# Performance work log

Measured on AMD Instinct MI355X. Metric: run time of the kernel, lower is better.

Reference implementation:

```python
import jax, jax.numpy as jnp
import numpy as np

N_NODES = 50000
N_EDGES = 800000
IN_CH = 64
HID = 64
HID2 = HID // 2  # 32


def _sage_conv(x, src, dst, w_l, w_r, b, n_nodes):
    """PyG SAGEConv (aggr='mean', root_weight=True):
    out = lin_l(mean_{j in N(i)} x_j) + lin_r(x_i), bias in lin_l.
    Messages flow src -> dst (source_to_target)."""
    msg = x[src]  # [E, d] gather of source features
    summed = jax.ops.segment_sum(msg, dst, num_segments=n_nodes)  # [N, d]
    cnt = jax.ops.segment_sum(jnp.ones((src.shape[0],), x.dtype), dst,
                              num_segments=n_nodes)  # [N]
    mean = summed / jnp.maximum(cnt, 1.0)[:, None]
    return mean @ w_l + b + x @ w_r


def setup_inputs() -> dict:
    key = jax.random.key(0)
    ks = jax.random.split(key, 12)
    s = 0.05
    x = jax.random.normal(ks[0], (N_NODES, IN_CH), dtype=jnp.float32)
    edge_index = jax.random.randint(ks[1], (2, N_EDGES), 0, N_NODES, dtype=jnp.int32)
    return {
        "x": x,
        "edge_index": edge_index,
        # SAGEConv layer 1 (in -> hidden)
        "w1_l": jax.random.normal(ks[2], (IN_CH, HID), dtype=jnp.float32) * s,
        "w1_r": jax.random.normal(ks[3], (IN_CH, HID), dtype=jnp.float32) * s,
        "b1": jnp.zeros((HID,), jnp.float32),
        # SAGEConv layer 2 (hidden -> hidden//2)
        "w2_l": jax.random.normal(ks[4], (HID, HID2), dtype=jnp.float32) * s,
        "w2_r": jax.random.normal(ks[5], (HID, HID2), dtype=jnp.float32) * s,
        "b2": jnp.zeros((HID2,), jnp.float32),
        # classifier MLP: Linear(32,16) -> ReLU -> Linear(16,2)
        "wc1": jax.random.normal(ks[6], (HID2, 16), dtype=jnp.float32) * s,
        "bc1": jnp.zeros((16,), jnp.float32),
        "wc2": jax.random.normal(ks[7], (16, 2), dtype=jnp.float32) * s,
        "bc2": jnp.zeros((2,), jnp.float32),
    }


def reference(x, edge_index, w1_l, w1_r, b1, w2_l, w2_r, b2, wc1, bc1, wc2, bc2):
    src, dst = edge_index[0], edge_index[1]
    n = x.shape[0]
    # Dropout is identity in eval / deterministic reference.
    h = jax.nn.relu(_sage_conv(x, src, dst, w1_l, w1_r, b1, n))
    h = jax.nn.relu(_sage_conv(h, src, dst, w2_l, w2_r, b2, n))
    h = jax.nn.relu(h @ wc1 + bc1)
    out = h @ wc2 + bc2  # [N, 2]
    return out
```

## Files before the change

### kernel.cpp

```cpp
#include <hip/hip_runtime.h>
#include <hip/hip_fp16.h>

#define N_NODES 50000
#define N_EDGES 800000
#define NBINS   391
#define CAP     4096
#define EPB     4096
#define NBLK_E  ((N_EDGES + EPB - 1) / EPB)
#define NTILE   391
#define LSTRIDE 129

__global__ __launch_bounds__(512) void k_binA(const int* __restrict__ src,
                                              const int* __restrict__ dst,
                                              int* __restrict__ bincur,
                                              int* __restrict__ binned) {
    __shared__ int cnt[NBINS];
    __shared__ int sc[512];
    __shared__ int lpos[NBINS];
    __shared__ int base[NBINS];
    __shared__ int stage[EPB];
    __shared__ unsigned short sbin[EPB];
    int t = threadIdx.x;
    int blkbase = blockIdx.x * EPB;
    int nE = min(EPB, N_EDGES - blkbase);
    for (int i = t; i < NBINS; i += 512) cnt[i] = 0;
    __syncthreads();
    int sv[8], dv[8];
#pragma unroll
    for (int k = 0; k < 8; ++k) {
        int e = blkbase + t + k * 512;
        if (e < N_EDGES) {
            sv[k] = src[e];
            dv[k] = dst[e];
            atomicAdd(&cnt[dv[k] >> 7], 1);
        } else dv[k] = -1;
    }
    __syncthreads();
    sc[t] = (t < NBINS) ? cnt[t] : 0;
    __syncthreads();
    for (int d = 1; d < 512; d <<= 1) {
        int add = (t >= d) ? sc[t - d] : 0;
        __syncthreads();
        sc[t] += add;
        __syncthreads();
    }
    for (int b = t; b < NBINS; b += 512) {
        int excl = sc[b] - cnt[b];
        lpos[b] = excl;
        sc[b] = excl;
        if (cnt[b] > 0) base[b] = b * CAP + atomicAdd(&bincur[b], cnt[b]);
    }
    __syncthreads();
#pragma unroll
    for (int k = 0; k < 8; ++k) {
        if (dv[k] >= 0) {
            int b = dv[k] >> 7;
            int p = atomicAdd(&lpos[b], 1);
            stage[p] = (sv[k] & 0xFFFF) | ((dv[k] & 127) << 16);
            sbin[p] = (unsigned short)b;
        }
    }
    __syncthreads();
    for (int i = t; i < nE; i += 512) {
        int b = sbin[i];
        int pos = base[b] + (i - sc[b]);
        if (pos < (b + 1) * CAP) binned[pos] = stage[i];
    }
}

__global__ __launch_bounds__(512) void k_binB_pre1(
        const int* __restrict__ bincur, int* __restrict__ binned,
        int* __restrict__ off, unsigned short* __restrict__ deg,
        int* __restrict__ esrc,
        const float* __restrict__ x,
        const float* __restrict__ wl, const float* __restrict__ wr,
        const float* __restrict__ b,
        __half* __restrict__ ph, float* __restrict__ q) {
    __shared__ float smem[64 * LSTRIDE];
    int t = threadIdx.x;
    int bb = blockIdx.x;
    if (bb < NBINS) {
        int* buf = (int*)smem;
        int* cnt = buf + CAP;
        int* tmp = cnt + 128;
        int* cur = tmp + 128;
        int n0 = bb << 7;
        int seg0 = bb * CAP;
        int n = min(bincur[bb], CAP);
        if (t < 128) cnt[t] = 0;
        __syncthreads();
        for (int i = t; i < n; i += 512) atomicAdd(&cnt[binned[seg0 + i] >> 16], 1);
        __syncthreads();
        int v = (t < 128) ? cnt[t] : 0;
        if (t < 128) tmp[t] = v;
        __syncthreads();
        int val = v;
        for (int d = 1; d < 128; d <<= 1) {
            int add = (t >= d && t < 128) ? tmp[t - d] : 0;
            __syncthreads();
            if (t < 128) { val += add; tmp[t] = val; }
            __syncthreads();
        }
        if (t < 128) {
            int excl = val - v;
            cur[t] = excl;
            int node = n0 + t;
            if (node < N_NODES) {
                off[node] = seg0 + excl;
                deg[node] = (unsigned short)v;
            }
        }
        __syncthreads();
        for (int i = t; i < n; i += 512) {
            int w = binned[seg0 + i];
            int p = atomicAdd(&cur[w >> 16], 1);
            buf[p] = w & 0xFFFF;
        }
        __syncthreads();
        for (int i = t; i < n; i += 512) esrc[seg0 + i] = buf[i];
        return;
    }
    float* sx = smem;
    int g0 = (bb - NBINS) * 128;
#pragma unroll
    for (int i = 0; i < 4; ++i) {
        int f = t + i * 512;
        int nd = f >> 4, cq = f & 15;
        int gn = g0 + nd;
        float4 v = (gn < N_NODES) ? ((const float4*)x)[(size_t)gn * 16 + cq]
                                  : make_float4(0.f, 0.f, 0.f, 0.f);
        sx[(cq * 4 + 0) * LSTRIDE + nd] = v.x;
        sx[(cq * 4 + 1) * LSTRIDE + nd] = v.y;
        sx[(cq * 4 + 2) * LSTRIDE + nd] = v.z;
        sx[(cq * 4 + 3) * LSTRIDE + nd] = v.w;
    }
    __syncthreads();
    int role = __builtin_amdgcn_readfirstlane(t >> 7);
    int wsel = role >> 1;
    int c0 = (role & 1) * 32;
    int ln = t & 127;
    int node = g0 + ln;
    const float* __restrict__ wm = wsel ? wr : wl;
    float acc[32];
    if (wsel) {
#pragma unroll
        for (int c = 0; c < 32; ++c) acc[c] = b[c0 + c];
    } else {
#pragma unroll
        for (int c = 0; c < 32; ++c) acc[c] = 0.f;
    }
#pragma unroll
    for (int k = 0; k < 64; ++k) {
        float xk = sx[k * LSTRIDE + ln];
#pragma unroll
        for (int c = 0; c < 32; ++c)
            acc[c] = fmaf(xk, wm[k * 64 + c0 + c], acc[c]);
    }
    if (node >= N_NODES) return;
    if (wsel == 0) {
        alignas(16) __half2 hv[16];
#pragma unroll
        for (int i = 0; i < 16; ++i)
            hv[i] = __floats2half2_rn(acc[2 * i], acc[2 * i + 1]);
        float4* op = (float4*)(ph + (size_t)node * 64 + c0);
#pragma unroll
        for (int i = 0; i < 4; ++i) op[i] = ((float4*)hv)[i];
    } else {
        float4* op = (float4*)(q + (size_t)node * 64 + c0);
#pragma unroll
        for (int i = 0; i < 8; ++i)
            op[i] = make_float4(acc[4 * i], acc[4 * i + 1], acc[4 * i + 2], acc[4 * i + 3]);
    }
}

__device__ __forceinline__ void acc8(float* a, float4 rv) {
    const __half2* hp = (const __half2*)&rv;
    float2 f0 = __half22float2(hp[0]), f1 = __half22float2(hp[1]);
    float2 f2 = __half22float2(hp[2]), f3 = __half22float2(hp[3]);
    a[0] += f0.x; a[1] += f0.y; a[2] += f1.x; a[3] += f1.y;
    a[4] += f2.x; a[5] += f2.y; a[6] += f3.x; a[7] += f3.y;
}

__global__ __launch_bounds__(1024) void k_agg1_pre2(
        const int* __restrict__ off, const unsigned short* __restrict__ deg,
        const int* __restrict__ esrc,
        const __half* __restrict__ ph, const float* __restrict__ q,
        const float* __restrict__ w2l, const float* __restrict__ w2r,
        const float* __restrict__ b2,
        __half* __restrict__ zh, float* __restrict__ r) {
    __shared__ float sx[64 * LSTRIDE];
    int t = threadIdx.x;
    int n0 = blockIdx.x << 7;
    int half = t >> 5;
    int l32 = t & 31;
    int eg = l32 >> 3;
    int cg = l32 & 7;
    for (int p = 0; p < 4; ++p) {
        int nl = half + 32 * p;
        int node = n0 + nl;
        if (node < N_NODES) {
            int s0 = off[node];
            int dv = deg[node];
            int s1 = s0 + dv;
            float a0[8] = {0,0,0,0,0,0,0,0}, a1[8] = {0,0,0,0,0,0,0,0};
            float a2[8] = {0,0,0,0,0,0,0,0}, a3[8] = {0,0,0,0,0,0,0,0};
            for (int i = s0; i < s1; i += 16) {
                int i0 = i + eg, i1 = i + 4 + eg, i2 = i + 8 + eg, i3 = i + 12 + eg;
                if (i0 < s1) acc8(a0, *(const float4*)(ph + (size_t)esrc[i0] * 64 + (cg << 3)));
                if (i1 < s1) acc8(a1, *(const float4*)(ph + (size_t)esrc[i1] * 64 + (cg << 3)));
                if (i2 < s1) acc8(a2, *(const float4*)(ph + (size_t)esrc[i2] * 64 + (cg << 3)));
                if (i3 < s1) acc8(a3, *(const float4*)(ph + (size_t)esrc[i3] * 64 + (cg << 3)));
            }
#pragma unroll
            for (int j = 0; j < 8; ++j) a0[j] += a1[j] + (a2[j] + a3[j]);
#pragma unroll
            for (int j = 0; j < 8; ++j) {
                a0[j] += __shfl_xor(a0[j], 8);
                a0[j] += __shfl_xor(a0[j], 16);
            }
            if (eg == 0) {
                float inv = 1.0f / fmaxf((float)dv, 1.0f);
                const float4* qp = (const float4*)(q + (size_t)node * 64 + (cg << 3));
                float4 q0 = qp[0], q1 = qp[1];
                float* d = sx + (cg << 3) * LSTRIDE + nl;
                d[0 * LSTRIDE] = fmaxf(fmaf(a0[0], inv, q0.x), 0.f);
                d[1 * LSTRIDE] = fmaxf(fmaf(a0[1], inv, q0.y), 0.f);
                d[2 * LSTRIDE] = fmaxf(fmaf(a0[2], inv, q0.z), 0.f);
                d[3 * LSTRIDE] = fmaxf(fmaf(a0[3], inv, q0.w), 0.f);
                d[4 * LSTRIDE] = fmaxf(fmaf(a0[4], inv, q1.x), 0.f);
                d[5 * LSTRIDE] = fmaxf(fmaf(a0[5], inv, q1.y), 0.f);
                d[6 * LSTRIDE] = fmaxf(fmaf(a0[6], inv, q1.z), 0.f);
                d[7 * LSTRIDE] = fmaxf(fmaf(a0[7], inv, q1.w), 0.f);
            }
        }
    }
    __syncthreads();
    int g = __builtin_amdgcn_readfirstlane(t >> 7);
    int role = g & 1;
    int c0 = (g >> 1) * 8;
    int ln = t & 127;
    int node = n0 + ln;
    const float* __restrict__ wm = role ? w2r : w2l;
    float acc[8];
    if (role) {
#pragma unroll
        for (int c = 0; c < 8; ++c) acc[c] = b2[c0 + c];
    } else {
#pragma unroll
        for (int c = 0; c < 8; ++c) acc[c] = 0.f;
    }
#pragma unroll
    for (int k = 0; k < 64; ++k) {
        float xk = sx[k * LSTRIDE + ln];
#pragma unroll
        for (int c = 0; c < 8; ++c)
            acc[c] = fmaf(xk, wm[k * 32 + c0 + c], acc[c]);
    }
    if (node >= N_NODES) return;
    if (role == 0) {
        alignas(16) __half2 hv[4];
#pragma unroll
        for (int i = 0; i < 4; ++i)
            hv[i] = __floats2half2_rn(acc[2 * i], acc[2 * i + 1]);
        *(float4*)(zh + (size_t)node * 32 + c0) = *(float4*)hv;
    } else {
        float4* op = (float4*)(r + (size_t)node * 32 + c0);
        op[0] = make_float4(acc[0], acc[1], acc[2], acc[3]);
        op[1] = make_float4(acc[4], acc[5], acc[6], acc[7]);
    }
}

__global__ __launch_bounds__(256) void k_agg2cls(const int* __restrict__ off,
                                                 const unsigned short* __restrict__ deg,
                                                 const int* __restrict__ esrc,
                                                 const __half* __restrict__ zh,
                                                 const float* __restrict__ r,
                                                 const float* __restrict__ wc1,
                                                 const float* __restrict__ bc1,
                                                 const float* __restrict__ wc2,
                                                 const float* __restrict__ bc2,
                                                 float* __restrict__ out) {
    __shared__ float sh2[16 * 33];
    __shared__ float sh3[16 * 17];
    __shared__ float swc1[512];
    __shared__ float sbc1[16];
    __shared__ float swc2[32];
    __shared__ float sbc2[2];
    int t = threadIdx.x;
    swc1[t] = wc1[t];
    swc1[t + 256] = wc1[t + 256];
    if (t < 16) sbc1[t] = bc1[t];
    if (t < 32) swc2[t] = wc2[t];
    if (t < 2)  sbc2[t] = bc2[t];

    int lane = t & 63;
    int l16 = lane & 15;
    int nl = (t >> 4) & 15;
    int node = blockIdx.x * 16 + nl;
    int eg = l16 >> 2;
    int cg = l16 & 3;
    int s0 = off[node];
    int dv = deg[node];
    int s1 = s0 + dv;
    float a0[8] = {0,0,0,0,0,0,0,0}, a1[8] = {0,0,0,0,0,0,0,0};
    float a2[8] = {0,0,0,0,0,0,0,0}, a3[8] = {0,0,0,0,0,0,0,0};
    for (int i = s0; i < s1; i += 16) {
        int i0 = i + eg, i1 = i + 4 + eg, i2 = i + 8 + eg, i3 = i + 12 + eg;
        if (i0 < s1) acc8(a0, *(const float4*)(zh + (size_t)esrc[i0] * 32 + (cg << 3)));
        if (i1 < s1) acc8(a1, *(const float4*)(zh + (size_t)esrc[i1] * 32 + (cg << 3)));
        if (i2 < s1) acc8(a2, *(const float4*)(zh + (size_t)esrc[i2] * 32 + (cg << 3)));
        if (i3 < s1) acc8(a3, *(const float4*)(zh + (size_t)esrc[i3] * 32 + (cg << 3)));
    }
#pragma unroll
    for (int j = 0; j < 8; ++j) a0[j] += a1[j] + (a2[j] + a3[j]);
#pragma unroll
    for (int j = 0; j < 8; ++j) {
        a0[j] += __shfl_xor(a0[j], 4);
        a0[j] += __shfl_xor(a0[j], 8);
    }
    if (eg == 0) {
        float inv = 1.0f / fmaxf((float)dv, 1.0f);
        const float4* rp = (const float4*)(r + (size_t)node * 32 + (cg << 3));
        float4 r0 = rp[0], r1 = rp[1];
        float* d = sh2 + nl * 33 + (cg << 3);
        d[0] = fmaxf(fmaf(a0[0], inv, r0.x), 0.f);
        d[1] = fmaxf(fmaf(a0[1], inv, r0.y), 0.f);
        d[2] = fmaxf(fmaf(a0[2], inv, r0.z), 0.f);
        d[3] = fmaxf(fmaf(a0[3], inv, r0.w), 0.f);
        d[4] = fmaxf(fmaf(a0[4], inv, r1.x), 0.f);
        d[5] = fmaxf(fmaf(a0[5], inv, r1.y), 0.f);
        d[6] = fmaxf(fmaf(a0[6], inv, r1.z), 0.f);
        d[7] = fmaxf(fmaf(a0[7], inv, r1.w), 0.f);
    }
    __syncthreads();
    int n = t >> 4, j = t & 15;
    float acc1 = sbc1[j];
#pragma unroll
    for (int k = 0; k < 32; ++k)
        acc1 = fmaf(sh2[n * 33 + k], swc1[k * 16 + j], acc1);
    sh3[n * 17 + j] = fmaxf(acc1, 0.f);
    __syncthreads();
    if (t < 16) {
        int nn = t;
        float o0 = sbc2[0], o1 = sbc2[1];
#pragma unroll
        for (int k = 0; k < 16; ++k) {
            float h3k = sh3[nn * 17 + k];
            o0 = fmaf(h3k, swc2[k * 2 + 0], o0);
            o1 = fmaf(h3k, swc2[k * 2 + 1], o1);
        }
        int gnode = blockIdx.x * 16 + nn;
        *(float2*)(out + (size_t)gnode * 2) = make_float2(o0, o1);
    }
}

extern "C" void kernel_launch(void* const* d_in, const int* in_sizes, int n_in,
                              void* d_out, int out_size, void* d_ws, size_t ws_size,
                              hipStream_t stream) {
    const float* x   = (const float*)d_in[0];
    const int*   ei  = (const int*)d_in[1];
    const int*   src = ei;
    const int*   dst = ei + N_EDGES;
    const float* w1l = (const float*)d_in[2];
    const float* w1r = (const float*)d_in[3];
    const float* b1  = (const float*)d_in[4];
    const float* w2l = (const float*)d_in[5];
    const float* w2r = (const float*)d_in[6];
    const float* b2  = (const float*)d_in[7];
    const float* wc1 = (const float*)d_in[8];
    const float* bc1 = (const float*)d_in[9];
    const float* wc2 = (const float*)d_in[10];
    const float* bc2 = (const float*)d_in[11];
    float* out = (float*)d_out;

    int*   wi     = (int*)d_ws;
    int*   bincur = wi;
    int*   binned = wi + 400;
    int*   esrc   = binned + (size_t)NBINS * CAP;
    int*   off    = esrc + (size_t)NBINS * CAP;
    unsigned short* deg = (unsigned short*)(off + N_NODES);
    float* q      = (float*)(deg + N_NODES + (N_NODES & 1));
    float* phf    = q + (size_t)64 * N_NODES;
    __half* ph    = (__half*)phf;
    float* zhf    = phf + (size_t)32 * N_NODES;
    __half* zh    = (__half*)zhf;
    float* r      = zhf + (size_t)16 * N_NODES;

    hipMemsetAsync(bincur, 0, 400 * sizeof(int), stream);
    k_binA<<<NBLK_E, 512, 0, stream>>>(src, dst, bincur, binned);

    k_binB_pre1<<<NBINS + NTILE, 512, 0, stream>>>(bincur, binned, off, deg, esrc,
                                                   x, w1l, w1r, b1, ph, q);

    k_agg1_pre2<<<NBINS, 1024, 0, stream>>>(off, deg, esrc, ph, q,
                                            w2l, w2r, b2, zh, r);

    k_agg2cls<<<N_NODES / 16, 256, 0, stream>>>(off, deg, esrc, zh, r,
                                                wc1, bc1, wc2, bc2, out);
}
```

Measured before the change: 187.5 us.

## Split layer-1 fp16 features into two 32-channel planes and gather per plane

The fp16 projected features are now stored as two separate planes of 32 channels each (64 bytes per node) instead of one 128-byte row. The aggregation kernel runs two phases, one per plane, so each phase's random gather touches a smaller working set that fits better in cache. Each node now gets 8 edges in flight per 32-lane group instead of 4. The cost is that the edge index list and offsets are read twice, plus an extra barrier and a three-step shuffle reduction per node.

```diff
diff --git a/kernel.cpp b/kernel.cpp
--- a/kernel.cpp
+++ b/kernel.cpp
@@ -75,7 +75,8 @@
         const float* __restrict__ x,
         const float* __restrict__ wl, const float* __restrict__ wr,
         const float* __restrict__ b,
-        __half* __restrict__ ph, float* __restrict__ q) {
+        __half* __restrict__ ph0, __half* __restrict__ ph1,
+        float* __restrict__ q) {
     __shared__ float smem[64 * LSTRIDE];
     int t = threadIdx.x;
     int bb = blockIdx.x;
@@ -162,7 +163,8 @@
 #pragma unroll
         for (int i = 0; i < 16; ++i)
             hv[i] = __floats2half2_rn(acc[2 * i], acc[2 * i + 1]);
-        float4* op = (float4*)(ph + (size_t)node * 64 + c0);
+        __half* plane = c0 ? ph1 : ph0;
+        float4* op = (float4*)(plane + (size_t)node * 32);
 #pragma unroll
         for (int i = 0; i < 4; ++i) op[i] = ((float4*)hv)[i];
     } else {
@@ -184,7 +186,8 @@
 __global__ __launch_bounds__(1024) void k_agg1_pre2(
         const int* __restrict__ off, const unsigned short* __restrict__ deg,
         const int* __restrict__ esrc,
-        const __half* __restrict__ ph, const float* __restrict__ q,
+        const __half* __restrict__ ph0, const __half* __restrict__ ph1,
+        const float* __restrict__ q,
         const float* __restrict__ w2l, const float* __restrict__ w2r,
         const float* __restrict__ b2,
         __half* __restrict__ zh, float* __restrict__ r) {
@@ -193,48 +196,51 @@
     int n0 = blockIdx.x << 7;
     int half = t >> 5;
     int l32 = t & 31;
-    int eg = l32 >> 3;
-    int cg = l32 & 7;
-    for (int p = 0; p < 4; ++p) {
-        int nl = half + 32 * p;
-        int node = n0 + nl;
-        if (node < N_NODES) {
-            int s0 = off[node];
-            int dv = deg[node];
-            int s1 = s0 + dv;
-            float a0[8] = {0,0,0,0,0,0,0,0}, a1[8] = {0,0,0,0,0,0,0,0};
-            float a2[8] = {0,0,0,0,0,0,0,0}, a3[8] = {0,0,0,0,0,0,0,0};
-            for (int i = s0; i < s1; i += 16) {
-                int i0 = i + eg, i1 = i + 4 + eg, i2 = i + 8 + eg, i3 = i + 12 + eg;
-                if (i0 < s1) acc8(a0, *(const float4*)(ph + (size_t)esrc[i0] * 64 + (cg << 3)));
-                if (i1 < s1) acc8(a1, *(const float4*)(ph + (size_t)esrc[i1] * 64 + (cg << 3)));
-                if (i2 < s1) acc8(a2, *(const float4*)(ph + (size_t)esrc[i2] * 64 + (cg << 3)));
-                if (i3 < s1) acc8(a3, *(const float4*)(ph + (size_t)esrc[i3] * 64 + (cg << 3)));
+    int eg = l32 >> 2;
+    int cg = l32 & 3;
+#pragma unroll
+    for (int phase = 0; phase < 2; ++phase) {
+        const __half* pp = phase ? ph1 : ph0;
+        for (int p = 0; p < 4; ++p) {
+            int nl = half + 32 * p;
+            int node = n0 + nl;
+            if (node < N_NODES) {
+                int s0 = off[node];
+                int dv = deg[node];
+                int s1 = s0 + dv;
+                float a0[8] = {0,0,0,0,0,0,0,0}, a1[8] = {0,0,0,0,0,0,0,0};
+                for (int i = s0; i < s1; i += 16) {
+                    int i0 = i + eg, i1 = i + 8 + eg;
+                    if (i0 < s1) acc8(a0, *(const float4*)(pp + (size_t)esrc[i0] * 32 + (cg << 3)));
+                    if (i1 < s1) acc8(a1, *(const float4*)(pp + (size_t)esrc[i1] * 32 + (cg << 3)));
+                }
+#pragma unroll
+                for (int j = 0; j < 8; ++j) a0[j] += a1[j];
+#pragma unroll
+                for (int j = 0; j < 8; ++j) {
+                    a0[j] += __shfl_xor(a0[j], 4);
+                    a0[j] += __shfl_xor(a0[j], 8);
+                    a0[j] += __shfl_xor(a0[j], 16);
+                }
+                if (eg == 0) {
+                    float inv = 1.0f / fmaxf((float)dv, 1.0f);
+                    int cb = phase * 32 + (cg << 3);
+                    const float4* qp = (const float4*)(q + (size_t)node * 64 + cb);
+                    float4 q0 = qp[0], q1 = qp[1];
+                    float* d = sx + cb * LSTRIDE + nl;
+                    d[0 * LSTRIDE] = fmaxf(fmaf(a0[0], inv, q0.x), 0.f);
+                    d[1 * LSTRIDE] = fmaxf(fmaf(a0[1], inv, q0.y), 0.f);
+                    d[2 * LSTRIDE] = fmaxf(fmaf(a0[2], inv, q0.z), 0.f);
+                    d[3 * LSTRIDE] = fmaxf(fmaf(a0[3], inv, q0.w), 0.f);
+                    d[4 * LSTRIDE] = fmaxf(fmaf(a0[4], inv, q1.x), 0.f);
+                    d[5 * LSTRIDE] = fmaxf(fmaf(a0[5], inv, q1.y), 0.f);
+                    d[6 * LSTRIDE] = fmaxf(fmaf(a0[6], inv, q1.z), 0.f);
+                    d[7 * LSTRIDE] = fmaxf(fmaf(a0[7], inv, q1.w), 0.f);
+                }
             }
-#pragma unroll
-            for (int j = 0; j < 8; ++j) a0[j] += a1[j] + (a2[j] + a3[j]);
-#pragma unroll
-            for (int j = 0; j < 8; ++j) {
-                a0[j] += __shfl_xor(a0[j], 8);
-                a0[j] += __shfl_xor(a0[j], 16);
-            }
-            if (eg == 0) {
-                float inv = 1.0f / fmaxf((float)dv, 1.0f);
-                const float4* qp = (const float4*)(q + (size_t)node * 64 + (cg << 3));
-                float4 q0 = qp[0], q1 = qp[1];
-                float* d = sx + (cg << 3) * LSTRIDE + nl;
-                d[0 * LSTRIDE] = fmaxf(fmaf(a0[0], inv, q0.x), 0.f);
-                d[1 * LSTRIDE] = fmaxf(fmaf(a0[1], inv, q0.y), 0.f);
-                d[2 * LSTRIDE] = fmaxf(fmaf(a0[2], inv, q0.z), 0.f);
-                d[3 * LSTRIDE] = fmaxf(fmaf(a0[3], inv, q0.w), 0.f);
-                d[4 * LSTRIDE] = fmaxf(fmaf(a0[4], inv, q1.x), 0.f);
-                d[5 * LSTRIDE] = fmaxf(fmaf(a0[5], inv, q1.y), 0.f);
-                d[6 * LSTRIDE] = fmaxf(fmaf(a0[6], inv, q1.z), 0.f);
-                d[7 * LSTRIDE] = fmaxf(fmaf(a0[7], inv, q1.w), 0.f);
-            }
-        }
-    }
-    __syncthreads();
+        }
+        __syncthreads();
+    }
     int g = __builtin_amdgcn_readfirstlane(t >> 7);
     int role = g & 1;
     int c0 = (g >> 1) * 8;
@@ -380,9 +386,11 @@
     int*   off    = esrc + (size_t)NBINS * CAP;
     unsigned short* deg = (unsigned short*)(off + N_NODES);
     float* q      = (float*)(deg + N_NODES + (N_NODES & 1));
-    float* phf    = q + (size_t)64 * N_NODES;
-    __half* ph    = (__half*)phf;
-    float* zhf    = phf + (size_t)32 * N_NODES;
+    float* p0f    = q + (size_t)64 * N_NODES;
+    __half* ph0   = (__half*)p0f;
+    float* p1f    = p0f + (size_t)16 * N_NODES;
+    __half* ph1   = (__half*)p1f;
+    float* zhf    = p1f + (size_t)16 * N_NODES;
     __half* zh    = (__half*)zhf;
     float* r      = zhf + (size_t)16 * N_NODES;
 
@@ -390,9 +398,9 @@
     k_binA<<<NBLK_E, 512, 0, stream>>>(src, dst, bincur, binned);
 
     k_binB_pre1<<<NBINS + NTILE, 512, 0, stream>>>(bincur, binned, off, deg, esrc,
-                                                   x, w1l, w1r, b1, ph, q);
-
-    k_agg1_pre2<<<NBINS, 1024, 0, stream>>>(off, deg, esrc, ph, q,
+                                                   x, w1l, w1r, b1, ph0, ph1, q);
+
+    k_agg1_pre2<<<NBINS, 1024, 0, stream>>>(off, deg, esrc, ph0, ph1, q,
                                             w2l, w2r, b2, zh, r);
 
     k_agg2cls<<<N_NODES / 16, 256, 0, stream>>>(off, deg, esrc, zh, r,
```

Measured after the change: 203.1 us. +8.3%, slower.

## Fuse first-layer projection into edge binning kernel, split bin finalize out

Applied to the files above, without the earlier changes.

The layer-1 dense projection (x@W_l, x@W_r) moves from the bin-finalize kernel into the first binning kernel as extra blocks, and bin finalize becomes its own kernel. The projection work now overlaps with the edge counting and scatter pass instead of with the per-bin sort. The intent is to balance the two launches better, since the binning pass is short and light on compute. The number of launches stays the same, and the binning blocks now reserve the larger shared-memory footprint of the projection, which may lower their occupancy.

```diff
diff --git a/kernel.cpp b/kernel.cpp
--- a/kernel.cpp
+++ b/kernel.cpp
@@ -10,68 +10,9 @@
 #define NTILE   391
 #define LSTRIDE 129
 
-__global__ __launch_bounds__(512) void k_binA(const int* __restrict__ src,
-                                              const int* __restrict__ dst,
-                                              int* __restrict__ bincur,
-                                              int* __restrict__ binned) {
-    __shared__ int cnt[NBINS];
-    __shared__ int sc[512];
-    __shared__ int lpos[NBINS];
-    __shared__ int base[NBINS];
-    __shared__ int stage[EPB];
-    __shared__ unsigned short sbin[EPB];
-    int t = threadIdx.x;
-    int blkbase = blockIdx.x * EPB;
-    int nE = min(EPB, N_EDGES - blkbase);
-    for (int i = t; i < NBINS; i += 512) cnt[i] = 0;
-    __syncthreads();
-    int sv[8], dv[8];
-#pragma unroll
-    for (int k = 0; k < 8; ++k) {
-        int e = blkbase + t + k * 512;
-        if (e < N_EDGES) {
-            sv[k] = src[e];
-            dv[k] = dst[e];
-            atomicAdd(&cnt[dv[k] >> 7], 1);
-        } else dv[k] = -1;
-    }
-    __syncthreads();
-    sc[t] = (t < NBINS) ? cnt[t] : 0;
-    __syncthreads();
-    for (int d = 1; d < 512; d <<= 1) {
-        int add = (t >= d) ? sc[t - d] : 0;
-        __syncthreads();
-        sc[t] += add;
-        __syncthreads();
-    }
-    for (int b = t; b < NBINS; b += 512) {
-        int excl = sc[b] - cnt[b];
-        lpos[b] = excl;
-        sc[b] = excl;
-        if (cnt[b] > 0) base[b] = b * CAP + atomicAdd(&bincur[b], cnt[b]);
-    }
-    __syncthreads();
-#pragma unroll
-    for (int k = 0; k < 8; ++k) {
-        if (dv[k] >= 0) {
-            int b = dv[k] >> 7;
-            int p = atomicAdd(&lpos[b], 1);
-            stage[p] = (sv[k] & 0xFFFF) | ((dv[k] & 127) << 16);
-            sbin[p] = (unsigned short)b;
-        }
-    }
-    __syncthreads();
-    for (int i = t; i < nE; i += 512) {
-        int b = sbin[i];
-        int pos = base[b] + (i - sc[b]);
-        if (pos < (b + 1) * CAP) binned[pos] = stage[i];
-    }
-}
-
-__global__ __launch_bounds__(512) void k_binB_pre1(
-        const int* __restrict__ bincur, int* __restrict__ binned,
-        int* __restrict__ off, unsigned short* __restrict__ deg,
-        int* __restrict__ esrc,
+__global__ __launch_bounds__(512) void k_binA_pre1(
+        const int* __restrict__ src, const int* __restrict__ dst,
+        int* __restrict__ bincur, int* __restrict__ binned,
         const float* __restrict__ x,
         const float* __restrict__ wl, const float* __restrict__ wr,
         const float* __restrict__ b,
@@ -79,49 +20,62 @@
     __shared__ float smem[64 * LSTRIDE];
     int t = threadIdx.x;
     int bb = blockIdx.x;
-    if (bb < NBINS) {
-        int* buf = (int*)smem;
-        int* cnt = buf + CAP;
-        int* tmp = cnt + 128;
-        int* cur = tmp + 128;
-        int n0 = bb << 7;
-        int seg0 = bb * CAP;
-        int n = min(bincur[bb], CAP);
-        if (t < 128) cnt[t] = 0;
-        __syncthreads();
-        for (int i = t; i < n; i += 512) atomicAdd(&cnt[binned[seg0 + i] >> 16], 1);
-        __syncthreads();
-        int v = (t < 128) ? cnt[t] : 0;
-        if (t < 128) tmp[t] = v;
-        __syncthreads();
-        int val = v;
-        for (int d = 1; d < 128; d <<= 1) {
-            int add = (t >= d && t < 128) ? tmp[t - d] : 0;
+    if (bb < NBLK_E) {
+        int* cnt  = (int*)smem;
+        int* sc   = cnt + 392;
+        int* lpos = sc + 512;
+        int* base = lpos + 392;
+        int* stage = base + 392;
+        unsigned short* sbin = (unsigned short*)(stage + EPB);
+        int blkbase = bb * EPB;
+        int nE = min(EPB, N_EDGES - blkbase);
+        for (int i = t; i < NBINS; i += 512) cnt[i] = 0;
+        __syncthreads();
+        int sv[8], dv[8];
+#pragma unroll
+        for (int k = 0; k < 8; ++k) {
+            int e = blkbase + t + k * 512;
+            if (e < N_EDGES) {
+                sv[k] = src[e];
+                dv[k] = dst[e];
+                atomicAdd(&cnt[dv[k] >> 7], 1);
+            } else dv[k] = -1;
+        }
+        __syncthreads();
+        sc[t] = (t < NBINS) ? cnt[t] : 0;
+        __syncthreads();
+        for (int d = 1; d < 512; d <<= 1) {
+            int add = (t >= d) ? sc[t - d] : 0;
             __syncthreads();
-            if (t < 128) { val += add; tmp[t] = val; }
+            sc[t] += add;
             __syncthreads();
         }
-        if (t < 128) {
-            int excl = val - v;
-            cur[t] = excl;
-            int node = n0 + t;
-            if (node < N_NODES) {
-                off[node] = seg0 + excl;
-                deg[node] = (unsigned short)v;
+        for (int bi = t; bi < NBINS; bi += 512) {
+            int excl = sc[bi] - cnt[bi];
+            lpos[bi] = excl;
+            sc[bi] = excl;
+            if (cnt[bi] > 0) base[bi] = bi * CAP + atomicAdd(&bincur[bi], cnt[bi]);
+        }
+        __syncthreads();
+#pragma unroll
+        for (int k = 0; k < 8; ++k) {
+            if (dv[k] >= 0) {
+                int bi = dv[k] >> 7;
+                int p = atomicAdd(&lpos[bi], 1);
+                stage[p] = (sv[k] & 0xFFFF) | ((dv[k] & 127) << 16);
+                sbin[p] = (unsigned short)bi;
             }
         }
         __syncthreads();
-        for (int i = t; i < n; i += 512) {
-            int w = binned[seg0 + i];
-            int p = atomicAdd(&cur[w >> 16], 1);
-            buf[p] = w & 0xFFFF;
-        }
-        __syncthreads();
-        for (int i = t; i < n; i += 512) esrc[seg0 + i] = buf[i];
+        for (int i = t; i < nE; i += 512) {
+            int bi = sbin[i];
+            int pos = base[bi] + (i - sc[bi]);
+            if (pos < (bi + 1) * CAP) binned[pos] = stage[i];
+        }
         return;
     }
     float* sx = smem;
-    int g0 = (bb - NBINS) * 128;
+    int g0 = (bb - NBLK_E) * 128;
 #pragma unroll
     for (int i = 0; i < 4; ++i) {
         int f = t + i * 512;
@@ -171,6 +125,52 @@
         for (int i = 0; i < 8; ++i)
             op[i] = make_float4(acc[4 * i], acc[4 * i + 1], acc[4 * i + 2], acc[4 * i + 3]);
     }
+}
+
+__global__ __launch_bounds__(512) void k_binB(const int* __restrict__ bincur,
+                                              const int* __restrict__ binned,
+                                              int* __restrict__ off,
+                                              unsigned short* __restrict__ deg,
+                                              int* __restrict__ esrc) {
+    __shared__ int buf[CAP];
+    __shared__ int cnt[128];
+    __shared__ int tmp[128];
+    __shared__ int cur[128];
+    int bb = blockIdx.x, t = threadIdx.x;
+    int n0 = bb << 7;
+    int seg0 = bb * CAP;
+    int n = min(bincur[bb], CAP);
+    if (t < 128) cnt[t] = 0;
+    __syncthreads();
+    for (int i = t; i < n; i += 512) atomicAdd(&cnt[binned[seg0 + i] >> 16], 1);
+    __syncthreads();
+    int v = (t < 128) ? cnt[t] : 0;
+    if (t < 128) tmp[t] = v;
+    __syncthreads();
+    int val = v;
+    for (int d = 1; d < 128; d <<= 1) {
+        int add = (t >= d && t < 128) ? tmp[t - d] : 0;
+        __syncthreads();
+        if (t < 128) { val += add; tmp[t] = val; }
+        __syncthreads();
+    }
+    if (t < 128) {
+        int excl = val - v;
+        cur[t] = excl;
+        int node = n0 + t;
+        if (node < N_NODES) {
+            off[node] = seg0 + excl;
+            deg[node] = (unsigned short)v;
+        }
+    }
+    __syncthreads();
+    for (int i = t; i < n; i += 512) {
+        int w = binned[seg0 + i];
+        int p = atomicAdd(&cur[w >> 16], 1);
+        buf[p] = w & 0xFFFF;
+    }
+    __syncthreads();
+    for (int i = t; i < n; i += 512) esrc[seg0 + i] = buf[i];
 }
 
 __device__ __forceinline__ void acc8(float* a, float4 rv) {
@@ -387,10 +387,10 @@
     float* r      = zhf + (size_t)16 * N_NODES;
 
     hipMemsetAsync(bincur, 0, 400 * sizeof(int), stream);
-    k_binA<<<NBLK_E, 512, 0, stream>>>(src, dst, bincur, binned);
-
-    k_binB_pre1<<<NBINS + NTILE, 512, 0, stream>>>(bincur, binned, off, deg, esrc,
-                                                   x, w1l, w1r, b1, ph, q);
+    k_binA_pre1<<<NBLK_E + NTILE, 512, 0, stream>>>(src, dst, bincur, binned,
+                                                    x, w1l, w1r, b1, ph, q);
+
+    k_binB<<<NBINS, 512, 0, stream>>>(bincur, binned, off, deg, esrc);
 
     k_agg1_pre2<<<NBINS, 1024, 0, stream>>>(off, deg, esrc, ph, q,
                                             w2l, w2r, b2, zh, r);
```

Result: faster. 183.7 us (-2.0%).
